# Performance work log

Hardware: AMD Instinct MI355X
Metric: run time of the kernel (lower is better)

The kernel has to match this reference:

```python
import jax, jax.numpy as jnp
import numpy as np
from jax import lax

B, CIN, H, W = 4, 720, 128, 128
MID = 512           # conv3x3 output channels (hardcoded in OCRHead)
KC, VC, NC = 256, 256, 19
BN_EPS = 1e-5


def setup_inputs() -> dict:
    key = jax.random.key(0)
    ks = jax.random.split(key, 16)
    s = 0.02
    f32 = jnp.float32
    return {
        "feats": jax.random.normal(ks[0], (B, CIN, H, W), f32),
        # conv3x3 (no bias)
        "w3": (jax.random.normal(ks[1], (MID, CIN, 3, 3), f32) * s),
        # BatchNorm affine params
        "gamma": 1.0 + 0.1 * jax.random.normal(ks[2], (MID,), f32),
        "beta": 0.1 * jax.random.normal(ks[3], (MID,), f32),
        # aux 1x1 conv (with bias)
        "aux_w": jax.random.normal(ks[4], (NC, MID), f32) * s,
        "aux_b": 0.01 * jax.random.normal(ks[5], (NC,), f32),
        # ObjectAttention: query 1x1 conv (no bias), key/value Linear (with bias), out 1x1 conv (no bias)
        "q_w": jax.random.normal(ks[6], (KC, MID), f32) * s,
        "k_w": jax.random.normal(ks[7], (KC, MID), f32) * s,
        "k_b": 0.01 * jax.random.normal(ks[8], (KC,), f32),
        "v_w": jax.random.normal(ks[9], (VC, MID), f32) * s,
        "v_b": 0.01 * jax.random.normal(ks[10], (VC,), f32),
        "out_w": jax.random.normal(ks[11], (MID, VC), f32) * s,
        # cls 1x1 conv (with bias)
        "cls_w": jax.random.normal(ks[12], (NC, MID), f32) * s,
        "cls_b": 0.01 * jax.random.normal(ks[13], (NC,), f32),
    }


def reference(feats, w3, gamma, beta, aux_w, aux_b, q_w, k_w, k_b, v_w, v_b, out_w, cls_w, cls_b):
    # conv3x3, padding=1, no bias
    x = lax.conv_general_dilated(feats, w3, window_strides=(1, 1),
                                 padding=((1, 1), (1, 1)),
                                 dimension_numbers=("NCHW", "OIHW", "NCHW"))
    # BatchNorm (batch mode: stats over batch+spatial) + relu
    mean = jnp.mean(x, axis=(0, 2, 3))
    var = jnp.var(x, axis=(0, 2, 3))
    x = (x - mean[None, :, None, None]) * lax.rsqrt(var + BN_EPS)[None, :, None, None]
    x = x * gamma[None, :, None, None] + beta[None, :, None, None]
    x = jax.nn.relu(x)

    # aux head: 1x1 conv with bias -> [B, K, H, W]
    aux_logits = jnp.einsum("bchw,kc->bkhw", x, aux_w) + aux_b[None, :, None, None]

    # SpatialGather: softmax over classes per pixel, normalize over pixels per class
    x_flat = x.reshape(B, MID, H * W).transpose(0, 2, 1)           # [B, N, C]
    probs = jax.nn.softmax(aux_logits.reshape(B, NC, H * W).transpose(0, 2, 1), axis=-1)  # [B, N, K]
    weights = probs / jnp.clip(jnp.sum(probs, axis=1, keepdims=True), 1e-6)
    context = jnp.einsum("bnk,bnc->bkc", weights, x_flat)          # [B, K, C]

    # ObjectAttention
    q = jnp.einsum("bchw,dc->bdhw", x, q_w).reshape(B, KC, H * W).transpose(0, 2, 1)  # [B, N, KC]
    k = jnp.einsum("bkc,dc->bkd", context, k_w) + k_b              # [B, K, KC]
    v = jnp.einsum("bkc,dc->bkd", context, v_w) + v_b              # [B, K, VC]
    scale = 1.0 / jnp.sqrt(jnp.asarray(KC, jnp.float32))
    attn = jax.nn.softmax(jnp.einsum("bnd,bkd->bnk", q * scale, k), axis=-1)  # [B, N, K]
    agg = jnp.einsum("bnk,bkv->bnv", attn, v)                      # [B, N, VC]
    agg_chw = agg.reshape(B, H, W, VC).transpose(0, 3, 1, 2)       # [B, VC, H, W]
    obj = jnp.einsum("bvhw,ov->bohw", agg_chw, out_w)              # [B, MID, H, W]

    x = x + obj
    logits = jnp.einsum("bchw,kc->bkhw", x, cls_w) + cls_b[None, :, None, None]
    return (logits, aux_logits)
```

## Files before the change

### kernel.cpp

```cpp
#include <hip/hip_runtime.h>
#include <hip/hip_bf16.h>


__device__ __forceinline__ float u_lo(unsigned u) { return __uint_as_float(u << 16); }
__device__ __forceinline__ float u_hi(unsigned u) { return __uint_as_float(u & 0xffff0000u); }
__device__ __forceinline__ float scrub(float v) { return isfinite(v) ? v : 1e4f; }
#define BF2F(h) __bfloat162float(h)

typedef __attribute__((ext_vector_type(8))) short bf16x8;
typedef __attribute__((ext_vector_type(4))) float f32x4;

#define SO_APACK  0ull
#define TAIL0     9371648ull
#define TA_AUXWT  (TAIL0 + 0ull)
#define TA_CLSWT  (TAIL0 + 38912ull)
#define TA_SS     (TAIL0 + 77824ull)
#define TA_PSUM   (TAIL0 + 81920ull)
#define TA_CTX    (TAIL0 + 82432ull)
#define TA_KMAT   (TAIL0 + 238080ull)
#define TA_VMAT   (TAIL0 + 315904ull)
#define TA_FCLS   (TAIL0 + 393728ull)
#define TA_MT     (TAIL0 + 413184ull)
#define TA_G      (TAIL0 + 568832ull)
#define TA_BNACC  (TAIL0 + 574608ull)

#define LDS_CI   40
#define LDS_ROW  (3 * LDS_CI)
#define LDS_TOT  (130 * LDS_ROW)

__global__ __launch_bounds__(256) void prep_small_kernel(
    const float* __restrict__ aux_w, const float* __restrict__ cls_w,
    float* __restrict__ aux_wt, float* __restrict__ cls_wt) {
  int i = blockIdx.x * 256 + threadIdx.x;
  if (i < 9728) {
    int k = i >> 9, c = i & 511;
    aux_wt[c * 19 + k] = aux_w[i];
    cls_wt[c * 19 + k] = cls_w[i];
  }
}

__global__ __launch_bounds__(256) void prep_apack_kernel(
    const float* __restrict__ w3, __hip_bfloat16* __restrict__ Apack) {
  int idx = blockIdx.x * 256 + threadIdx.x;
  if (idx >= 512 * 736) return;
  int oc = idx / 736, ci = idx - (idx / 736) * 736;
  float v[9];
#pragma unroll
  for (int k = 0; k < 9; ++k) v[k] = 0.f;
  if (ci < 720) {
    const float* src = w3 + ((size_t)oc * 720 + ci) * 9;
#pragma unroll
    for (int k = 0; k < 9; ++k) v[k] = src[k];
  }
#pragma unroll
  for (int k = 0; k < 9; ++k)
    Apack[((size_t)k * 512 + oc) * 736 + ci] = __float2bfloat16(v[k]);
}

__global__ __launch_bounds__(256) void conv_mfma_kernel(
    const float* __restrict__ feats, const __hip_bfloat16* __restrict__ Apack,
    __hip_bfloat16* __restrict__ X) {
  __shared__ short Blds[LDS_TOT];
  int bid = blockIdx.x;
  int xcd = bid & 7;
  int slot = bid >> 3;
  int oc_t = slot & 3;
  int gx = (slot >> 2) * 8 + xcd;
  int b = gx >> 7, h = gx & 127;
  int tid = threadIdx.x;
  int wave = tid >> 6, lane = tid & 63;
  int wm = wave >> 1, wn = wave & 1;
  int l15 = lane & 15, quad = lane >> 4;

  f32x4 acc[4][4];
#pragma unroll
  for (int mb = 0; mb < 4; ++mb)
#pragma unroll
    for (int nb = 0; nb < 4; ++nb) acc[mb][nb] = (f32x4){0.f, 0.f, 0.f, 0.f};

  for (int i = tid; i < 2 * LDS_ROW; i += 256) {
    int wp = (i < LDS_ROW) ? 0 : 129;
    Blds[wp * LDS_ROW + (i < LDS_ROW ? i : i - LDS_ROW)] = 0;
  }

  const short* Ab = (const short*)Apack;
  int oc_row = oc_t * 128 + wm * 64 + l15;

  const float* fbase = feats + (((size_t)b * 720) << 14) + lane * 2;

  float2 pre[3][8];
  {
    int ci0 = wave * 8;
#pragma unroll
    for (int r = 0; r < 3; ++r) {
      int hr = h - 1 + r;
#pragma unroll
      for (int j = 0; j < 8; ++j) pre[r][j] = (float2){0.f, 0.f};
      if ((unsigned)hr < 128u) {
        const float* p = fbase + ((size_t)ci0 << 14) + hr * 128;
#pragma unroll
        for (int j = 0; j < 8; ++j)
          pre[r][j] = *reinterpret_cast<const float2*>(p + (size_t)j * 16384);
      }
    }
  }

  for (int cb = 0; cb < 23; ++cb) {
    __syncthreads();
#pragma unroll
    for (int r = 0; r < 3; ++r) {
      union { bf16x8 v; __hip_bfloat16 hh[8]; } E, O;
#pragma unroll
      for (int j = 0; j < 8; ++j) {
        E.hh[j] = __float2bfloat16(pre[r][j].x);
        O.hh[j] = __float2bfloat16(pre[r][j].y);
      }
      short* wb = &Blds[(lane * 2 + 1) * LDS_ROW + r * LDS_CI + wave * 8];
      *reinterpret_cast<bf16x8*>(wb) = E.v;
      *reinterpret_cast<bf16x8*>(wb + LDS_ROW) = O.v;
    }
    __syncthreads();
    if (cb < 22) {
      int ci0 = (cb + 1) * 32 + wave * 8;
      bool civ = (ci0 < 720);
#pragma unroll
      for (int r = 0; r < 3; ++r) {
        int hr = h - 1 + r;
#pragma unroll
        for (int j = 0; j < 8; ++j) pre[r][j] = (float2){0.f, 0.f};
        if (civ && ((unsigned)hr < 128u)) {
          const float* p = fbase + ((size_t)ci0 << 14) + hr * 128;
#pragma unroll
          for (int j = 0; j < 8; ++j)
            pre[r][j] = *reinterpret_cast<const float2*>(p + (size_t)j * 16384);
        }
      }
    }
#pragma unroll
    for (int r = 0; r < 3; ++r) {
#pragma unroll
      for (int dw = 0; dw < 3; ++dw) {
        int plane = r * 3 + dw;
        const short* ap = Ab + ((size_t)plane * 512 + oc_row) * 736 + cb * 32 + quad * 8;
        bf16x8 af[4];
#pragma unroll
        for (int mb = 0; mb < 4; ++mb)
          af[mb] = *(const bf16x8*)(ap + (size_t)mb * 16 * 736);
        bf16x8 bfr[4];
#pragma unroll
        for (int nb = 0; nb < 4; ++nb) {
          int px = wn * 64 + nb * 16 + l15;
          bfr[nb] = *(const bf16x8*)(&Blds[(px + dw) * LDS_ROW + r * LDS_CI + quad * 8]);
        }
#pragma unroll
        for (int mb = 0; mb < 4; ++mb)
#pragma unroll
          for (int nb = 0; nb < 4; ++nb)
            acc[mb][nb] = __builtin_amdgcn_mfma_f32_16x16x32_bf16(
                af[mb], bfr[nb], acc[mb][nb], 0, 0, 0);
      }
    }
  }
#pragma unroll
  for (int nb = 0; nb < 4; ++nb) {
    int px = wn * 64 + nb * 16 + l15;
    __hip_bfloat16* xr = X + (((size_t)b * 16384 + h * 128 + px) << 9);
#pragma unroll
    for (int mb = 0; mb < 4; ++mb) {
      int oc = oc_t * 128 + wm * 64 + mb * 16 + quad * 4;
      union { unsigned long long u; __hip_bfloat16 hh[4]; } P;
      P.hh[0] = __float2bfloat16(acc[mb][nb][0]);
      P.hh[1] = __float2bfloat16(acc[mb][nb][1]);
      P.hh[2] = __float2bfloat16(acc[mb][nb][2]);
      P.hh[3] = __float2bfloat16(acc[mb][nb][3]);
      *reinterpret_cast<unsigned long long*>(xr + oc) = P.u;
    }
  }
}

__global__ __launch_bounds__(256) void bn_stats_kernel(
    const __hip_bfloat16* __restrict__ X, float* __restrict__ bnacc) {
  int row0 = blockIdx.x * 128;
  int c0 = threadIdx.x * 2;
  float s0 = 0.f, s1 = 0.f, q0 = 0.f, q1 = 0.f;
  const __hip_bfloat16* p = X + ((size_t)row0 << 9) + c0;
  for (int r = 0; r < 128; ++r) {
    unsigned u = *reinterpret_cast<const unsigned*>(p + ((size_t)r << 9));
    float f0 = u_lo(u), f1 = u_hi(u);
    s0 += f0; q0 += f0 * f0;
    s1 += f1; q1 += f1 * f1;
  }
  atomicAdd(&bnacc[c0], s0);
  atomicAdd(&bnacc[c0 + 1], s1);
  atomicAdd(&bnacc[512 + c0], q0);
  atomicAdd(&bnacc[512 + c0 + 1], q1);
}

__global__ __launch_bounds__(256) void bn_finalize_kernel(
    const float* __restrict__ bnacc, const float* __restrict__ gamma,
    const float* __restrict__ beta, float* __restrict__ ss_out) {
  int c = blockIdx.x * 256 + threadIdx.x;
  float mean = bnacc[c] * (1.f / 65536.f);
  float var = bnacc[512 + c] * (1.f / 65536.f) - mean * mean;
  float gi = gamma[c] * rsqrtf(var + 1e-5f);
  ss_out[c * 2] = gi;
  ss_out[c * 2 + 1] = beta[c] - mean * gi;
}

__global__ __launch_bounds__(256) void bn_apply_kernel(
    __hip_bfloat16* __restrict__ X, const float* __restrict__ ss) {
  __shared__ float ssl[1024];
  for (int i = threadIdx.x; i < 1024; i += 256) ssl[i] = ss[i];
  __syncthreads();
  size_t idx = ((size_t)blockIdx.x * 256 + threadIdx.x) * 8;
  int c0 = (int)(idx & 511);
  uint4 u = *reinterpret_cast<const uint4*>(X + idx);
  unsigned arr[4] = {u.x, u.y, u.z, u.w};
  union { uint4 u; __hip_bfloat16 h[8]; } O;
#pragma unroll
  for (int j = 0; j < 4; ++j) {
    int c = c0 + 2 * j;
    float f0 = fmaxf(fmaf(u_lo(arr[j]), ssl[2 * c], ssl[2 * c + 1]), 0.f);
    float f1 = fmaxf(fmaf(u_hi(arr[j]), ssl[2 * c + 2], ssl[2 * c + 3]), 0.f);
    O.h[2 * j] = __float2bfloat16(f0);
    O.h[2 * j + 1] = __float2bfloat16(f1);
  }
  *reinterpret_cast<uint4*>(X + idx) = O.u;
}

__global__ __launch_bounds__(256) void aux_ctx_kernel(
    const __hip_bfloat16* __restrict__ X, const float* __restrict__ aux_wt,
    const float* __restrict__ aux_b,
    float* __restrict__ ctx, float* __restrict__ psum,
    float* __restrict__ aux_out) {
  int b = blockIdx.y;
  int n0 = blockIdx.x * 256;
  int tid = threadIdx.x;
  __shared__ float pl[19][256];

  int p0 = n0 + tid;
  const __hip_bfloat16* xr = X + (((size_t)b * 16384 + p0) << 9);
  float a0[19];
#pragma unroll
  for (int k = 0; k < 19; ++k) a0[k] = aux_b[k];
  for (int c = 0; c < 512; c += 8) {
    uint4 u = *reinterpret_cast<const uint4*>(xr + c);
    unsigned w4[4] = {u.x, u.y, u.z, u.w};
#pragma unroll
    for (int j = 0; j < 4; ++j) {
      float f0 = u_lo(w4[j]), f1 = u_hi(w4[j]);
      const float* wr = aux_wt + (c + 2 * j) * 19;
#pragma unroll
      for (int k = 0; k < 19; ++k)
        a0[k] = fmaf(wr[19 + k], f1, fmaf(wr[k], f0, a0[k]));
    }
  }
  {
    size_t ob = ((size_t)b * 19) << 14;
#pragma unroll
    for (int k = 0; k < 19; ++k) {
      if (!(b == 3 && k >= 10))
        aux_out[ob + ((size_t)k << 14) + p0] = scrub(a0[k]);
    }
  }
  float mx0 = a0[0];
#pragma unroll
  for (int k = 1; k < 19; ++k) mx0 = fmaxf(mx0, a0[k]);
  float s0 = 0.f;
#pragma unroll
  for (int k = 0; k < 19; ++k) { a0[k] = __expf(a0[k] - mx0); s0 += a0[k]; }
  float r0 = 1.f / s0;
#pragma unroll
  for (int k = 0; k < 19; ++k) {
    float q0 = a0[k] * r0;
    pl[k][tid] = q0;
    a0[k] = q0;
  }
#pragma unroll
  for (int k = 0; k < 19; ++k) {
    float t = a0[k];
#pragma unroll
    for (int off = 32; off > 0; off >>= 1) t += __shfl_down(t, off);
    if ((tid & 63) == 0) atomicAdd(&psum[b * 19 + k], t);
  }
  __syncthreads();

  int c0 = tid * 2;
  const __hip_bfloat16* x2 = X + (((size_t)b * 16384 + n0) << 9) + c0;
  float b0[19], b1[19];
#pragma unroll
  for (int k = 0; k < 19; ++k) { b0[k] = 0.f; b1[k] = 0.f; }
  for (int nl = 0; nl < 256; ++nl) {
    unsigned u = *reinterpret_cast<const unsigned*>(x2 + ((size_t)nl << 9));
    float xv0 = u_lo(u), xv1 = u_hi(u);
#pragma unroll
    for (int kk = 0; kk < 19; ++kk) {
      float p = pl[kk][nl];
      b0[kk] = fmaf(p, xv0, b0[kk]);
      b1[kk] = fmaf(p, xv1, b1[kk]);
    }
  }
#pragma unroll
  for (int kk = 0; kk < 19; ++kk) {
    atomicAdd(&ctx[((b * 19 + kk) << 9) + c0], b0[kk]);
    atomicAdd(&ctx[((b * 19 + kk) << 9) + c0 + 1], b1[kk]);
  }
}

__global__ __launch_bounds__(256) void small_a_kernel(
    const float* __restrict__ ctx, const float* __restrict__ psum,
    const float* __restrict__ k_w, const float* __restrict__ k_b,
    const float* __restrict__ v_w, const float* __restrict__ v_b,
    const float* __restrict__ cls_w, const float* __restrict__ out_w,
    float* __restrict__ Kmat, float* __restrict__ vmat, float* __restrict__ fcls) {
  int i = blockIdx.x * 256 + threadIdx.x;
  if (i < 38912) {
    int half = i / 19456;
    int j = i - half * 19456;
    int d = j & 255;
    int t = j >> 8;
    const float* w = (half ? v_w : k_w) + d * 512;
    const float* cr = ctx + (t << 9);
    float s = 0.f;
    for (int c = 0; c < 512; ++c) s = fmaf(w[c], cr[c], s);
    float rcp = 1.f / fmaxf(psum[t], 1e-6f);
    float bias = (half ? v_b : k_b)[d];
    (half ? vmat : Kmat)[j] = s * rcp + bias;
  } else if (i < 43776) {
    int j = i - 38912;
    int vv = j & 255, k = j >> 8;
    const float* cw = cls_w + k * 512;
    float s = 0.f;
    for (int c = 0; c < 512; ++c) s = fmaf(cw[c], out_w[c * 256 + vv], s);
    fcls[j] = s;
  }
}

__global__ __launch_bounds__(256) void small_b_kernel(
    const float* __restrict__ Kmat, const float* __restrict__ vmat,
    const float* __restrict__ fcls, const float* __restrict__ q_w,
    float* __restrict__ m_t, float* __restrict__ g) {
  int i = blockIdx.x * 256 + threadIdx.x;
  if (i < 38912) {
    int kk = i % 19;
    int t = i / 19;
    int c = t & 511, b = t >> 9;
    const float* kr = Kmat + ((b * 19 + kk) << 8);
    float s = 0.f;
    for (int d = 0; d < 256; ++d) s = fmaf(q_w[d * 512 + c], kr[d], s);
    m_t[i] = s;
  } else if (i < 40356) {
    int j = i - 38912;
    int k = j % 19;
    int t = j / 19;
    const float* vr = vmat + (t << 8);
    const float* fr = fcls + (k << 8);
    float s = 0.f;
    for (int v = 0; v < 256; ++v) s = fmaf(fr[v], vr[v], s);
    g[j] = s;
  }
}

__global__ __launch_bounds__(256) void final_fused_kernel(
    const __hip_bfloat16* __restrict__ X, const float* __restrict__ m_t,
    const float* __restrict__ cls_wt, const float* __restrict__ cls_b,
    const float* __restrict__ g, float* __restrict__ out) {
  int b = blockIdx.y;
  int n = blockIdx.x * 256 + threadIdx.x;
  float macc[19], cacc[19];
#pragma unroll
  for (int k = 0; k < 19; ++k) { macc[k] = 0.f; cacc[k] = 0.f; }
  const __hip_bfloat16* xr = X + (((size_t)b * 16384 + n) << 9);
  for (int c = 0; c < 512; c += 8) {
    uint4 u = *reinterpret_cast<const uint4*>(xr + c);
    unsigned w4[4] = {u.x, u.y, u.z, u.w};
#pragma unroll
    for (int j = 0; j < 4; ++j) {
      float f0 = u_lo(w4[j]), f1 = u_hi(w4[j]);
      const float* mr = m_t + (size_t)(b * 512 + c + 2 * j) * 19;
      const float* wr = cls_wt + (c + 2 * j) * 19;
#pragma unroll
      for (int k = 0; k < 19; ++k) {
        macc[k] = fmaf(mr[19 + k], f1, fmaf(mr[k], f0, macc[k]));
        cacc[k] = fmaf(wr[19 + k], f1, fmaf(wr[k], f0, cacc[k]));
      }
    }
  }
  float mx = -1e30f;
#pragma unroll
  for (int k = 0; k < 19; ++k) { macc[k] *= 0.0625f; mx = fmaxf(mx, macc[k]); }
  float sum = 0.f;
#pragma unroll
  for (int k = 0; k < 19; ++k) { macc[k] = __expf(macc[k] - mx); sum += macc[k]; }
  float r = 1.f / sum;
#pragma unroll
  for (int k = 0; k < 19; ++k) cacc[k] += cls_b[k];
#pragma unroll
  for (int kk = 0; kk < 19; ++kk) {
    float av = macc[kk] * r;
    const float* gr = g + (b * 19 + kk) * 19;
#pragma unroll
    for (int k = 0; k < 19; ++k) cacc[k] = fmaf(gr[k], av, cacc[k]);
  }
  size_t ob = ((size_t)b * 19) << 14;
#pragma unroll
  for (int k = 0; k < 19; ++k)
    out[ob + ((size_t)k << 14) + n] = scrub(cacc[k]);
}

__global__ __launch_bounds__(256) void aux_tail_kernel(
    const __hip_bfloat16* __restrict__ X, const float* __restrict__ aux_w,
    const float* __restrict__ aux_b, float* __restrict__ aux_out) {
  __shared__ float wt[9728];
  for (int i = threadIdx.x; i < 9728; i += 256) {
    int k = i >> 9, c = i & 511;
    wt[c * 19 + k] = aux_w[i];
  }
  __syncthreads();
  const int b = 3;
  int n = blockIdx.x * 256 + threadIdx.x;
  float acc[19];
#pragma unroll
  for (int k = 0; k < 19; ++k) acc[k] = aux_b[k];
  const __hip_bfloat16* xr = X + (((size_t)b * 16384 + n) << 9);
  for (int c = 0; c < 512; c += 8) {
    uint4 u = *reinterpret_cast<const uint4*>(xr + c);
    unsigned w4[4] = {u.x, u.y, u.z, u.w};
#pragma unroll
    for (int j = 0; j < 4; ++j) {
      float f0 = u_lo(w4[j]), f1 = u_hi(w4[j]);
      const float* wr = &wt[(c + 2 * j) * 19];
#pragma unroll
      for (int k = 0; k < 19; ++k)
        acc[k] = fmaf(wr[19 + k], f1, fmaf(wr[k], f0, acc[k]));
    }
  }
  size_t ob = ((size_t)b * 19) << 14;
#pragma unroll
  for (int k = 10; k < 19; ++k)
    aux_out[ob + ((size_t)k << 14) + n] = scrub(acc[k]);
}

extern "C" void kernel_launch(void* const* d_in, const int* in_sizes, int n_in,
                              void* d_out, int out_size, void* d_ws, size_t ws_size,
                              hipStream_t stream) {
  const float* feats = (const float*)d_in[0];
  const float* w3    = (const float*)d_in[1];
  const float* gamma = (const float*)d_in[2];
  const float* beta  = (const float*)d_in[3];
  const float* aux_w = (const float*)d_in[4];
  const float* aux_b = (const float*)d_in[5];
  const float* q_w   = (const float*)d_in[6];
  const float* k_w   = (const float*)d_in[7];
  const float* k_b   = (const float*)d_in[8];
  const float* v_w   = (const float*)d_in[9];
  const float* v_b   = (const float*)d_in[10];
  const float* out_w = (const float*)d_in[11];
  const float* cls_w = (const float*)d_in[12];
  const float* cls_b = (const float*)d_in[13];

  float* logits_out = (float*)d_out;
  float* aux_out    = logits_out + 1245184;

  __hip_bfloat16* X = (__hip_bfloat16*)d_ws;

  char* ob = (char*)d_out;
  __hip_bfloat16* Apack = (__hip_bfloat16*)(ob + SO_APACK);
  float* aux_wt = (float*)(ob + TA_AUXWT);
  float* cls_wt = (float*)(ob + TA_CLSWT);
  float* ssbuf  = (float*)(ob + TA_SS);
  float* psum   = (float*)(ob + TA_PSUM);
  float* ctx    = (float*)(ob + TA_CTX);
  float* Kmat   = (float*)(ob + TA_KMAT);
  float* vmat   = (float*)(ob + TA_VMAT);
  float* fcls   = (float*)(ob + TA_FCLS);
  float* m_t    = (float*)(ob + TA_MT);
  float* g      = (float*)(ob + TA_G);
  float* bnacc  = (float*)(ob + TA_BNACC);

  hipMemsetAsync(ob + TA_PSUM, 0, 512 + 155648, stream);
  hipMemsetAsync(ob + TA_BNACC, 0, 4096, stream);

  prep_small_kernel<<<38, 256, 0, stream>>>(aux_w, cls_w, aux_wt, cls_wt);
  prep_apack_kernel<<<1472, 256, 0, stream>>>(w3, Apack);
  conv_mfma_kernel<<<2048, 256, 0, stream>>>(feats, Apack, X);
  bn_stats_kernel<<<512, 256, 0, stream>>>(X, bnacc);
  bn_finalize_kernel<<<2, 256, 0, stream>>>(bnacc, gamma, beta, ssbuf);
  bn_apply_kernel<<<16384, 256, 0, stream>>>(X, ssbuf);
  aux_ctx_kernel<<<dim3(64, 4), 256, 0, stream>>>(X, aux_wt, aux_b, ctx, psum, aux_out);
  small_a_kernel<<<171, 256, 0, stream>>>(ctx, psum, k_w, k_b, v_w, v_b, cls_w, out_w,
                                          Kmat, vmat, fcls);
  small_b_kernel<<<158, 256, 0, stream>>>(Kmat, vmat, fcls, q_w, m_t, g);
  final_fused_kernel<<<dim3(64, 4), 256, 0, stream>>>(X, m_t, cls_wt, cls_b, g, logits_out);
  aux_tail_kernel<<<64, 256, 0, stream>>>(X, aux_w, aux_b, aux_out);
}
```

Measured before the change: 1.453 ms.

## Fuse post-conv BN, aux, attention and classifier stages into one cooperative kernel

```diff
diff --git a/kernel.cpp b/kernel.cpp
--- a/kernel.cpp
+++ b/kernel.cpp
@@ -1,5 +1,8 @@
 #include <hip/hip_runtime.h>
 #include <hip/hip_bf16.h>
+#include <hip/hip_cooperative_groups.h>
+
+namespace cg = cooperative_groups;
 
 
 __device__ __forceinline__ float u_lo(unsigned u) { return __uint_as_float(u << 16); }
@@ -178,267 +181,263 @@
   }
 }
 
-__global__ __launch_bounds__(256) void bn_stats_kernel(
-    const __hip_bfloat16* __restrict__ X, float* __restrict__ bnacc) {
-  int row0 = blockIdx.x * 128;
-  int c0 = threadIdx.x * 2;
-  float s0 = 0.f, s1 = 0.f, q0 = 0.f, q1 = 0.f;
-  const __hip_bfloat16* p = X + ((size_t)row0 << 9) + c0;
-  for (int r = 0; r < 128; ++r) {
-    unsigned u = *reinterpret_cast<const unsigned*>(p + ((size_t)r << 9));
-    float f0 = u_lo(u), f1 = u_hi(u);
-    s0 += f0; q0 += f0 * f0;
-    s1 += f1; q1 += f1 * f1;
-  }
-  atomicAdd(&bnacc[c0], s0);
-  atomicAdd(&bnacc[c0 + 1], s1);
-  atomicAdd(&bnacc[512 + c0], q0);
-  atomicAdd(&bnacc[512 + c0 + 1], q1);
-}
-
-__global__ __launch_bounds__(256) void bn_finalize_kernel(
-    const float* __restrict__ bnacc, const float* __restrict__ gamma,
-    const float* __restrict__ beta, float* __restrict__ ss_out) {
-  int c = blockIdx.x * 256 + threadIdx.x;
-  float mean = bnacc[c] * (1.f / 65536.f);
-  float var = bnacc[512 + c] * (1.f / 65536.f) - mean * mean;
-  float gi = gamma[c] * rsqrtf(var + 1e-5f);
-  ss_out[c * 2] = gi;
-  ss_out[c * 2 + 1] = beta[c] - mean * gi;
-}
-
-__global__ __launch_bounds__(256) void bn_apply_kernel(
-    __hip_bfloat16* __restrict__ X, const float* __restrict__ ss) {
-  __shared__ float ssl[1024];
-  for (int i = threadIdx.x; i < 1024; i += 256) ssl[i] = ss[i];
+__global__ __launch_bounds__(256) void megatail_kernel(
+    __hip_bfloat16* __restrict__ X,
+    const float* __restrict__ gamma, const float* __restrict__ beta,
+    const float* __restrict__ aux_wt, const float* __restrict__ aux_b,
+    const float* __restrict__ aux_w, const float* __restrict__ cls_wt,
+    const float* __restrict__ cls_b,
+    const float* __restrict__ k_w, const float* __restrict__ k_b,
+    const float* __restrict__ v_w, const float* __restrict__ v_b,
+    const float* __restrict__ out_w, const float* __restrict__ cls_w,
+    const float* __restrict__ q_w,
+    float* __restrict__ ctx, float* __restrict__ psum,
+    float* __restrict__ bnacc,
+    float* __restrict__ Kmat, float* __restrict__ vmat,
+    float* __restrict__ fcls, float* __restrict__ m_t,
+    float* __restrict__ gmat,
+    float* __restrict__ logits_out, float* __restrict__ aux_out) {
+  cg::grid_group grid = cg::this_grid();
+  __shared__ float smem[10752];
+  float* ssl = smem;
+  float* pl  = smem + 1024;
+  float* wt  = smem + 1024;
+
+  int gq = blockIdx.x;
+  int tid = threadIdx.x;
+  int b = gq >> 6;
+  int n = (gq & 63) * 256 + tid;
+  size_t tile0 = ((size_t)b * 16384 + (gq & 63) * 256);
+
+  {
+    int c0 = tid * 2;
+    const __hip_bfloat16* p = X + (tile0 << 9) + c0;
+    float s0 = 0.f, s1 = 0.f, q0 = 0.f, q1 = 0.f;
+    for (int r = 0; r < 256; ++r) {
+      unsigned u = *reinterpret_cast<const unsigned*>(p + ((size_t)r << 9));
+      float f0 = u_lo(u), f1 = u_hi(u);
+      s0 += f0; q0 += f0 * f0;
+      s1 += f1; q1 += f1 * f1;
+    }
+    atomicAdd(&bnacc[c0], s0);
+    atomicAdd(&bnacc[c0 + 1], s1);
+    atomicAdd(&bnacc[512 + c0], q0);
+    atomicAdd(&bnacc[512 + c0 + 1], q1);
+  }
+  grid.sync();
+
+  {
+    int c0 = tid * 2;
+#pragma unroll
+    for (int t = 0; t < 2; ++t) {
+      int c = c0 + t;
+      float mean = bnacc[c] * (1.f / 65536.f);
+      float var = bnacc[512 + c] * (1.f / 65536.f) - mean * mean;
+      float gi = gamma[c] * rsqrtf(var + 1e-5f);
+      ssl[c * 2] = gi;
+      ssl[c * 2 + 1] = beta[c] - mean * gi;
+    }
+  }
   __syncthreads();
-  size_t idx = ((size_t)blockIdx.x * 256 + threadIdx.x) * 8;
-  int c0 = (int)(idx & 511);
-  uint4 u = *reinterpret_cast<const uint4*>(X + idx);
-  unsigned arr[4] = {u.x, u.y, u.z, u.w};
-  union { uint4 u; __hip_bfloat16 h[8]; } O;
-#pragma unroll
-  for (int j = 0; j < 4; ++j) {
-    int c = c0 + 2 * j;
-    float f0 = fmaxf(fmaf(u_lo(arr[j]), ssl[2 * c], ssl[2 * c + 1]), 0.f);
-    float f1 = fmaxf(fmaf(u_hi(arr[j]), ssl[2 * c + 2], ssl[2 * c + 3]), 0.f);
-    O.h[2 * j] = __float2bfloat16(f0);
-    O.h[2 * j + 1] = __float2bfloat16(f1);
-  }
-  *reinterpret_cast<uint4*>(X + idx) = O.u;
-}
-
-__global__ __launch_bounds__(256) void aux_ctx_kernel(
-    const __hip_bfloat16* __restrict__ X, const float* __restrict__ aux_wt,
-    const float* __restrict__ aux_b,
-    float* __restrict__ ctx, float* __restrict__ psum,
-    float* __restrict__ aux_out) {
-  int b = blockIdx.y;
-  int n0 = blockIdx.x * 256;
-  int tid = threadIdx.x;
-  __shared__ float pl[19][256];
-
-  int p0 = n0 + tid;
-  const __hip_bfloat16* xr = X + (((size_t)b * 16384 + p0) << 9);
-  float a0[19];
-#pragma unroll
-  for (int k = 0; k < 19; ++k) a0[k] = aux_b[k];
-  for (int c = 0; c < 512; c += 8) {
-    uint4 u = *reinterpret_cast<const uint4*>(xr + c);
-    unsigned w4[4] = {u.x, u.y, u.z, u.w};
-#pragma unroll
-    for (int j = 0; j < 4; ++j) {
-      float f0 = u_lo(w4[j]), f1 = u_hi(w4[j]);
-      const float* wr = aux_wt + (c + 2 * j) * 19;
-#pragma unroll
-      for (int k = 0; k < 19; ++k)
-        a0[k] = fmaf(wr[19 + k], f1, fmaf(wr[k], f0, a0[k]));
-    }
-  }
-  {
+
+  {
+    __hip_bfloat16* xr = X + (((size_t)b * 16384 + n) << 9);
+    float a0[19];
+#pragma unroll
+    for (int k = 0; k < 19; ++k) a0[k] = aux_b[k];
+    for (int c = 0; c < 512; c += 8) {
+      uint4 u = *reinterpret_cast<const uint4*>(xr + c);
+      unsigned arr[4] = {u.x, u.y, u.z, u.w};
+      union { uint4 u; __hip_bfloat16 h[8]; unsigned w[4]; } O;
+#pragma unroll
+      for (int j = 0; j < 4; ++j) {
+        int cc = c + 2 * j;
+        float f0 = fmaxf(fmaf(u_lo(arr[j]), ssl[2 * cc], ssl[2 * cc + 1]), 0.f);
+        float f1 = fmaxf(fmaf(u_hi(arr[j]), ssl[2 * cc + 2], ssl[2 * cc + 3]), 0.f);
+        O.h[2 * j] = __float2bfloat16(f0);
+        O.h[2 * j + 1] = __float2bfloat16(f1);
+        float g0 = u_lo(O.w[j]), g1 = u_hi(O.w[j]);
+        const float* wr = aux_wt + cc * 19;
+#pragma unroll
+        for (int k = 0; k < 19; ++k)
+          a0[k] = fmaf(wr[19 + k], g1, fmaf(wr[k], g0, a0[k]));
+      }
+      *reinterpret_cast<uint4*>(xr + c) = O.u;
+    }
     size_t ob = ((size_t)b * 19) << 14;
 #pragma unroll
     for (int k = 0; k < 19; ++k) {
       if (!(b == 3 && k >= 10))
-        aux_out[ob + ((size_t)k << 14) + p0] = scrub(a0[k]);
-    }
-  }
-  float mx0 = a0[0];
-#pragma unroll
-  for (int k = 1; k < 19; ++k) mx0 = fmaxf(mx0, a0[k]);
-  float s0 = 0.f;
-#pragma unroll
-  for (int k = 0; k < 19; ++k) { a0[k] = __expf(a0[k] - mx0); s0 += a0[k]; }
-  float r0 = 1.f / s0;
-#pragma unroll
-  for (int k = 0; k < 19; ++k) {
-    float q0 = a0[k] * r0;
-    pl[k][tid] = q0;
-    a0[k] = q0;
-  }
-#pragma unroll
-  for (int k = 0; k < 19; ++k) {
-    float t = a0[k];
-#pragma unroll
-    for (int off = 32; off > 0; off >>= 1) t += __shfl_down(t, off);
-    if ((tid & 63) == 0) atomicAdd(&psum[b * 19 + k], t);
+        aux_out[ob + ((size_t)k << 14) + n] = scrub(a0[k]);
+    }
+    float mx0 = a0[0];
+#pragma unroll
+    for (int k = 1; k < 19; ++k) mx0 = fmaxf(mx0, a0[k]);
+    float s0 = 0.f;
+#pragma unroll
+    for (int k = 0; k < 19; ++k) { a0[k] = __expf(a0[k] - mx0); s0 += a0[k]; }
+    float r0 = 1.f / s0;
+#pragma unroll
+    for (int k = 0; k < 19; ++k) {
+      float q0 = a0[k] * r0;
+      pl[k * 256 + tid] = q0;
+      a0[k] = q0;
+    }
+#pragma unroll
+    for (int k = 0; k < 19; ++k) {
+      float t = a0[k];
+#pragma unroll
+      for (int off = 32; off > 0; off >>= 1) t += __shfl_down(t, off);
+      if ((tid & 63) == 0) atomicAdd(&psum[b * 19 + k], t);
+    }
   }
   __syncthreads();
 
-  int c0 = tid * 2;
-  const __hip_bfloat16* x2 = X + (((size_t)b * 16384 + n0) << 9) + c0;
-  float b0[19], b1[19];
-#pragma unroll
-  for (int k = 0; k < 19; ++k) { b0[k] = 0.f; b1[k] = 0.f; }
-  for (int nl = 0; nl < 256; ++nl) {
-    unsigned u = *reinterpret_cast<const unsigned*>(x2 + ((size_t)nl << 9));
-    float xv0 = u_lo(u), xv1 = u_hi(u);
+  {
+    int c0 = tid * 2;
+    const __hip_bfloat16* x2 = X + (tile0 << 9) + c0;
+    float b0[19], b1[19];
+#pragma unroll
+    for (int k = 0; k < 19; ++k) { b0[k] = 0.f; b1[k] = 0.f; }
+    for (int nl = 0; nl < 256; ++nl) {
+      unsigned u = *reinterpret_cast<const unsigned*>(x2 + ((size_t)nl << 9));
+      float xv0 = u_lo(u), xv1 = u_hi(u);
+#pragma unroll
+      for (int kk = 0; kk < 19; ++kk) {
+        float p = pl[kk * 256 + nl];
+        b0[kk] = fmaf(p, xv0, b0[kk]);
+        b1[kk] = fmaf(p, xv1, b1[kk]);
+      }
+    }
 #pragma unroll
     for (int kk = 0; kk < 19; ++kk) {
-      float p = pl[kk][nl];
-      b0[kk] = fmaf(p, xv0, b0[kk]);
-      b1[kk] = fmaf(p, xv1, b1[kk]);
-    }
-  }
-#pragma unroll
-  for (int kk = 0; kk < 19; ++kk) {
-    atomicAdd(&ctx[((b * 19 + kk) << 9) + c0], b0[kk]);
-    atomicAdd(&ctx[((b * 19 + kk) << 9) + c0 + 1], b1[kk]);
-  }
-}
-
-__global__ __launch_bounds__(256) void small_a_kernel(
-    const float* __restrict__ ctx, const float* __restrict__ psum,
-    const float* __restrict__ k_w, const float* __restrict__ k_b,
-    const float* __restrict__ v_w, const float* __restrict__ v_b,
-    const float* __restrict__ cls_w, const float* __restrict__ out_w,
-    float* __restrict__ Kmat, float* __restrict__ vmat, float* __restrict__ fcls) {
-  int i = blockIdx.x * 256 + threadIdx.x;
-  if (i < 38912) {
-    int half = i / 19456;
-    int j = i - half * 19456;
-    int d = j & 255;
-    int t = j >> 8;
-    const float* w = (half ? v_w : k_w) + d * 512;
-    const float* cr = ctx + (t << 9);
-    float s = 0.f;
-    for (int c = 0; c < 512; ++c) s = fmaf(w[c], cr[c], s);
-    float rcp = 1.f / fmaxf(psum[t], 1e-6f);
-    float bias = (half ? v_b : k_b)[d];
-    (half ? vmat : Kmat)[j] = s * rcp + bias;
-  } else if (i < 43776) {
-    int j = i - 38912;
-    int vv = j & 255, k = j >> 8;
-    const float* cw = cls_w + k * 512;
-    float s = 0.f;
-    for (int c = 0; c < 512; ++c) s = fmaf(cw[c], out_w[c * 256 + vv], s);
-    fcls[j] = s;
-  }
-}
-
-__global__ __launch_bounds__(256) void small_b_kernel(
-    const float* __restrict__ Kmat, const float* __restrict__ vmat,
-    const float* __restrict__ fcls, const float* __restrict__ q_w,
-    float* __restrict__ m_t, float* __restrict__ g) {
-  int i = blockIdx.x * 256 + threadIdx.x;
-  if (i < 38912) {
-    int kk = i % 19;
-    int t = i / 19;
-    int c = t & 511, b = t >> 9;
-    const float* kr = Kmat + ((b * 19 + kk) << 8);
-    float s = 0.f;
-    for (int d = 0; d < 256; ++d) s = fmaf(q_w[d * 512 + c], kr[d], s);
-    m_t[i] = s;
-  } else if (i < 40356) {
-    int j = i - 38912;
-    int k = j % 19;
-    int t = j / 19;
-    const float* vr = vmat + (t << 8);
-    const float* fr = fcls + (k << 8);
-    float s = 0.f;
-    for (int v = 0; v < 256; ++v) s = fmaf(fr[v], vr[v], s);
-    g[j] = s;
-  }
-}
-
-__global__ __launch_bounds__(256) void final_fused_kernel(
-    const __hip_bfloat16* __restrict__ X, const float* __restrict__ m_t,
-    const float* __restrict__ cls_wt, const float* __restrict__ cls_b,
-    const float* __restrict__ g, float* __restrict__ out) {
-  int b = blockIdx.y;
-  int n = blockIdx.x * 256 + threadIdx.x;
-  float macc[19], cacc[19];
-#pragma unroll
-  for (int k = 0; k < 19; ++k) { macc[k] = 0.f; cacc[k] = 0.f; }
-  const __hip_bfloat16* xr = X + (((size_t)b * 16384 + n) << 9);
-  for (int c = 0; c < 512; c += 8) {
-    uint4 u = *reinterpret_cast<const uint4*>(xr + c);
-    unsigned w4[4] = {u.x, u.y, u.z, u.w};
-#pragma unroll
-    for (int j = 0; j < 4; ++j) {
-      float f0 = u_lo(w4[j]), f1 = u_hi(w4[j]);
-      const float* mr = m_t + (size_t)(b * 512 + c + 2 * j) * 19;
-      const float* wr = cls_wt + (c + 2 * j) * 19;
-#pragma unroll
-      for (int k = 0; k < 19; ++k) {
-        macc[k] = fmaf(mr[19 + k], f1, fmaf(mr[k], f0, macc[k]));
-        cacc[k] = fmaf(wr[19 + k], f1, fmaf(wr[k], f0, cacc[k]));
-      }
-    }
-  }
-  float mx = -1e30f;
-#pragma unroll
-  for (int k = 0; k < 19; ++k) { macc[k] *= 0.0625f; mx = fmaxf(mx, macc[k]); }
-  float sum = 0.f;
-#pragma unroll
-  for (int k = 0; k < 19; ++k) { macc[k] = __expf(macc[k] - mx); sum += macc[k]; }
-  float r = 1.f / sum;
-#pragma unroll
-  for (int k = 0; k < 19; ++k) cacc[k] += cls_b[k];
-#pragma unroll
-  for (int kk = 0; kk < 19; ++kk) {
-    float av = macc[kk] * r;
-    const float* gr = g + (b * 19 + kk) * 19;
-#pragma unroll
-    for (int k = 0; k < 19; ++k) cacc[k] = fmaf(gr[k], av, cacc[k]);
-  }
-  size_t ob = ((size_t)b * 19) << 14;
-#pragma unroll
-  for (int k = 0; k < 19; ++k)
-    out[ob + ((size_t)k << 14) + n] = scrub(cacc[k]);
-}
-
-__global__ __launch_bounds__(256) void aux_tail_kernel(
-    const __hip_bfloat16* __restrict__ X, const float* __restrict__ aux_w,
-    const float* __restrict__ aux_b, float* __restrict__ aux_out) {
-  __shared__ float wt[9728];
-  for (int i = threadIdx.x; i < 9728; i += 256) {
-    int k = i >> 9, c = i & 511;
-    wt[c * 19 + k] = aux_w[i];
-  }
-  __syncthreads();
-  const int b = 3;
-  int n = blockIdx.x * 256 + threadIdx.x;
-  float acc[19];
-#pragma unroll
-  for (int k = 0; k < 19; ++k) acc[k] = aux_b[k];
-  const __hip_bfloat16* xr = X + (((size_t)b * 16384 + n) << 9);
-  for (int c = 0; c < 512; c += 8) {
-    uint4 u = *reinterpret_cast<const uint4*>(xr + c);
-    unsigned w4[4] = {u.x, u.y, u.z, u.w};
-#pragma unroll
-    for (int j = 0; j < 4; ++j) {
-      float f0 = u_lo(w4[j]), f1 = u_hi(w4[j]);
-      const float* wr = &wt[(c + 2 * j) * 19];
-#pragma unroll
-      for (int k = 0; k < 19; ++k)
-        acc[k] = fmaf(wr[19 + k], f1, fmaf(wr[k], f0, acc[k]));
-    }
-  }
-  size_t ob = ((size_t)b * 19) << 14;
-#pragma unroll
-  for (int k = 10; k < 19; ++k)
-    aux_out[ob + ((size_t)k << 14) + n] = scrub(acc[k]);
+      atomicAdd(&ctx[((b * 19 + kk) << 9) + c0], b0[kk]);
+      atomicAdd(&ctx[((b * 19 + kk) << 9) + c0 + 1], b1[kk]);
+    }
+  }
+  grid.sync();
+
+  {
+    int i = gq * 256 + tid;
+    if (i < 38912) {
+      int half = i / 19456;
+      int j = i - half * 19456;
+      int d = j & 255;
+      int t = j >> 8;
+      const float* w = (half ? v_w : k_w) + d * 512;
+      const float* cr = ctx + (t << 9);
+      float s = 0.f;
+      for (int c = 0; c < 512; ++c) s = fmaf(w[c], cr[c], s);
+      float rcp = 1.f / fmaxf(psum[t], 1e-6f);
+      float bias = (half ? v_b : k_b)[d];
+      (half ? vmat : Kmat)[j] = s * rcp + bias;
+    } else if (i < 43776) {
+      int j = i - 38912;
+      int vv = j & 255, k = j >> 8;
+      const float* cw = cls_w + k * 512;
+      float s = 0.f;
+      for (int c = 0; c < 512; ++c) s = fmaf(cw[c], out_w[c * 256 + vv], s);
+      fcls[j] = s;
+    }
+  }
+  grid.sync();
+
+  {
+    int i = gq * 256 + tid;
+    if (i < 38912) {
+      int kk = i % 19;
+      int t = i / 19;
+      int c = t & 511, bb = t >> 9;
+      const float* kr = Kmat + ((bb * 19 + kk) << 8);
+      float s = 0.f;
+      for (int d = 0; d < 256; ++d) s = fmaf(q_w[d * 512 + c], kr[d], s);
+      m_t[i] = s;
+    } else if (i < 40356) {
+      int j = i - 38912;
+      int k = j % 19;
+      int t = j / 19;
+      const float* vr = vmat + (t << 8);
+      const float* fr = fcls + (k << 8);
+      float s = 0.f;
+      for (int v = 0; v < 256; ++v) s = fmaf(fr[v], vr[v], s);
+      gmat[j] = s;
+    }
+  }
+  grid.sync();
+
+  {
+    for (int i = tid; i < 9728; i += 256) wt[i] = cls_wt[i];
+    __syncthreads();
+    float macc[19], cacc[19];
+#pragma unroll
+    for (int k = 0; k < 19; ++k) { macc[k] = 0.f; cacc[k] = 0.f; }
+    const __hip_bfloat16* xr = X + (((size_t)b * 16384 + n) << 9);
+    for (int c = 0; c < 512; c += 8) {
+      uint4 u = *reinterpret_cast<const uint4*>(xr + c);
+      unsigned w4[4] = {u.x, u.y, u.z, u.w};
+#pragma unroll
+      for (int j = 0; j < 4; ++j) {
+        float f0 = u_lo(w4[j]), f1 = u_hi(w4[j]);
+        const float* mr = m_t + (size_t)(b * 512 + c + 2 * j) * 19;
+        const float* wr = &wt[(c + 2 * j) * 19];
+#pragma unroll
+        for (int k = 0; k < 19; ++k) {
+          macc[k] = fmaf(mr[19 + k], f1, fmaf(mr[k], f0, macc[k]));
+          cacc[k] = fmaf(wr[19 + k], f1, fmaf(wr[k], f0, cacc[k]));
+        }
+      }
+    }
+    float mx = -1e30f;
+#pragma unroll
+    for (int k = 0; k < 19; ++k) { macc[k] *= 0.0625f; mx = fmaxf(mx, macc[k]); }
+    float sum = 0.f;
+#pragma unroll
+    for (int k = 0; k < 19; ++k) { macc[k] = __expf(macc[k] - mx); sum += macc[k]; }
+    float r = 1.f / sum;
+#pragma unroll
+    for (int k = 0; k < 19; ++k) cacc[k] += cls_b[k];
+#pragma unroll
+    for (int kk = 0; kk < 19; ++kk) {
+      float av = macc[kk] * r;
+      const float* gr = gmat + (b * 19 + kk) * 19;
+#pragma unroll
+      for (int k = 0; k < 19; ++k) cacc[k] = fmaf(gr[k], av, cacc[k]);
+    }
+    size_t ob = ((size_t)b * 19) << 14;
+#pragma unroll
+    for (int k = 0; k < 19; ++k)
+      logits_out[ob + ((size_t)k << 14) + n] = scrub(cacc[k]);
+  }
+  grid.sync();
+
+  if (gq < 64) {
+    for (int i = tid; i < 9728; i += 256) {
+      int k = i >> 9, c = i & 511;
+      wt[c * 19 + k] = aux_w[i];
+    }
+    __syncthreads();
+    int nn = gq * 256 + tid;
+    float acc[19];
+#pragma unroll
+    for (int k = 0; k < 19; ++k) acc[k] = aux_b[k];
+    const __hip_bfloat16* xr = X + (((size_t)3 * 16384 + nn) << 9);
+    for (int c = 0; c < 512; c += 8) {
+      uint4 u = *reinterpret_cast<const uint4*>(xr + c);
+      unsigned w4[4] = {u.x, u.y, u.z, u.w};
+#pragma unroll
+      for (int j = 0; j < 4; ++j) {
+        float f0 = u_lo(w4[j]), f1 = u_hi(w4[j]);
+        const float* wr = &wt[(c + 2 * j) * 19];
+#pragma unroll
+        for (int k = 0; k < 19; ++k)
+          acc[k] = fmaf(wr[19 + k], f1, fmaf(wr[k], f0, acc[k]));
+      }
+    }
+    size_t ob = ((size_t)3 * 19) << 14;
+#pragma unroll
+    for (int k = 10; k < 19; ++k)
+      aux_out[ob + ((size_t)k << 14) + nn] = scrub(acc[k]);
+  }
 }
 
 extern "C" void kernel_launch(void* const* d_in, const int* in_sizes, int n_in,
@@ -468,14 +467,13 @@
   __hip_bfloat16* Apack = (__hip_bfloat16*)(ob + SO_APACK);
   float* aux_wt = (float*)(ob + TA_AUXWT);
   float* cls_wt = (float*)(ob + TA_CLSWT);
-  float* ssbuf  = (float*)(ob + TA_SS);
   float* psum   = (float*)(ob + TA_PSUM);
   float* ctx    = (float*)(ob + TA_CTX);
   float* Kmat   = (float*)(ob + TA_KMAT);
   float* vmat   = (float*)(ob + TA_VMAT);
   float* fcls   = (float*)(ob + TA_FCLS);
   float* m_t    = (float*)(ob + TA_MT);
-  float* g      = (float*)(ob + TA_G);
+  float* gmat   = (float*)(ob + TA_G);
   float* bnacc  = (float*)(ob + TA_BNACC);
 
   hipMemsetAsync(ob + TA_PSUM, 0, 512 + 155648, stream);
@@ -484,13 +482,15 @@
   prep_small_kernel<<<38, 256, 0, stream>>>(aux_w, cls_w, aux_wt, cls_wt);
   prep_apack_kernel<<<1472, 256, 0, stream>>>(w3, Apack);
   conv_mfma_kernel<<<2048, 256, 0, stream>>>(feats, Apack, X);
-  bn_stats_kernel<<<512, 256, 0, stream>>>(X, bnacc);
-  bn_finalize_kernel<<<2, 256, 0, stream>>>(bnacc, gamma, beta, ssbuf);
-  bn_apply_kernel<<<16384, 256, 0, stream>>>(X, ssbuf);
-  aux_ctx_kernel<<<dim3(64, 4), 256, 0, stream>>>(X, aux_wt, aux_b, ctx, psum, aux_out);
-  small_a_kernel<<<171, 256, 0, stream>>>(ctx, psum, k_w, k_b, v_w, v_b, cls_w, out_w,
-                                          Kmat, vmat, fcls);
-  small_b_kernel<<<158, 256, 0, stream>>>(Kmat, vmat, fcls, q_w, m_t, g);
-  final_fused_kernel<<<dim3(64, 4), 256, 0, stream>>>(X, m_t, cls_wt, cls_b, g, logits_out);
-  aux_tail_kernel<<<64, 256, 0, stream>>>(X, aux_w, aux_b, aux_out);
+
+  void* kargs[] = {
+    (void*)&X, (void*)&gamma, (void*)&beta, (void*)&aux_wt, (void*)&aux_b,
+    (void*)&aux_w, (void*)&cls_wt, (void*)&cls_b, (void*)&k_w, (void*)&k_b,
+    (void*)&v_w, (void*)&v_b, (void*)&out_w, (void*)&cls_w, (void*)&q_w,
+    (void*)&ctx, (void*)&psum, (void*)&bnacc, (void*)&Kmat, (void*)&vmat,
+    (void*)&fcls, (void*)&m_t, (void*)&gmat, (void*)&logits_out,
+    (void*)&aux_out
+  };
+  hipLaunchCooperativeKernel((const void*)megatail_kernel, dim3(256), dim3(256),
+                             kargs, 0, stream);
 }
```

Result: slower. 1.569 ms (+7.9%).
